# Kernel tuning notes

Hardware: AMD Instinct MI355X
Metric: run time of the kernel (lower is better)

The kernel has to match this reference:

```python
import jax, jax.numpy as jnp
import numpy as np

B, C, H, W = 4, 256, 64, 64
C8 = C // 8
MH, MW = 256, 256  # mask input resolution


def _conv(x, w, b, pad, dil=1):
    out = jax.lax.conv_general_dilated(
        x, w, window_strides=(1, 1),
        padding=[(pad, pad), (pad, pad)],
        rhs_dilation=(dil, dil),
        dimension_numbers=("NCHW", "OIHW", "NCHW"))
    return out + b[None, :, None, None]


def setup_inputs() -> dict:
    key = jax.random.key(0)
    ks = jax.random.split(key, 16)

    def w_init(k, shape):
        fan_in = shape[1] * shape[2] * shape[3]
        bound = 1.0 / np.sqrt(fan_in)
        return jax.random.uniform(k, shape, jnp.float32, -bound, bound)

    def b_init(k, n, fan_in):
        bound = 1.0 / np.sqrt(fan_in)
        return jax.random.uniform(k, (n,), jnp.float32, -bound, bound)

    return {
        "x": jax.random.normal(ks[0], (B, C, H, W), jnp.float32),
        "mask": jax.random.uniform(ks[1], (B, 1, MH, MW), jnp.float32),
        "w_ctx": w_init(ks[2], (C, C, 7, 7)),   "b_ctx": b_init(ks[3], C, C * 49),
        "w_wide": w_init(ks[4], (C, C, 5, 5)),  "b_wide": b_init(ks[5], C, C * 25),
        "w_comb": w_init(ks[6], (C, 2 * C, 1, 1)), "b_comb": b_init(ks[7], C, 2 * C),
        "w_q": w_init(ks[8], (C8, C, 1, 1)),    "b_q": b_init(ks[9], C8, C),
        "w_k": w_init(ks[10], (C8, C, 1, 1)),   "b_k": b_init(ks[11], C8, C),
        "w_v": w_init(ks[12], (C, C, 1, 1)),    "b_v": b_init(ks[13], C, C),
    }


def reference(x, mask, w_ctx, b_ctx, w_wide, b_wide, w_comb, b_comb,
              w_q, b_q, w_k, b_k, w_v, b_v):
    local_ctx = _conv(x, w_ctx, b_ctx, pad=3, dil=1)          # [B,C,H,W]
    wide_ctx = _conv(x, w_wide, b_wide, pad=6, dil=3)         # [B,C,H,W]
    multi = _conv(jnp.concatenate([local_ctx, wide_ctx], axis=1),
                  w_comb, b_comb, pad=0)                       # [B,C,H,W]

    b, c, h, w = multi.shape
    n = h * w
    q = _conv(multi, w_q, b_q, pad=0).reshape(b, C8, n)        # [B,C/8,N]
    k = _conv(multi, w_k, b_k, pad=0).reshape(b, C8, n)        # [B,C/8,N]
    v = _conv(multi, w_v, b_v, pad=0).reshape(b, c, n)         # [B,C,N]

    scores = jnp.einsum("bcm,bcn->bmn", q, k)                  # [B,N,N]
    attn = jax.nn.softmax(scores, axis=-1)
    out = jnp.einsum("bcn,bmn->bcm", v, attn).reshape(b, c, h, w)

    # nearest-neighbor resize of mask to (h, w), matching torch F.interpolate
    mh, mw = mask.shape[2], mask.shape[3]
    idx_h = (jnp.arange(h) * mh) // h
    idx_w = (jnp.arange(w) * mw) // w
    mask_r = mask[:, :, idx_h][:, :, :, idx_w]                 # [B,1,h,w]

    return out * (1.0 + mask_r)
```

## Files before the change

### kernel.cpp

```cpp
#include <hip/hip_runtime.h>
#include <math.h>

#define BB 4
#define CC 256
#define HH 64
#define WW 64
#define NN 4096

typedef _Float16 f16x8 __attribute__((ext_vector_type(8)));
typedef float f32x4 __attribute__((ext_vector_type(4)));

__device__ __forceinline__ void prep_pad(
    int blk, const float* __restrict__ x, _Float16* __restrict__ xpad)
{
  int pr = blk % 76;
  int b  = blk / 76;
  int ci = threadIdx.x;
  int r = pr - 6;
  _Float16* dst = xpad + (((size_t)b*76 + pr)*76)*256 + ci;
  if (r < 0 || r >= HH) {
    for (int pc = 0; pc < 76; ++pc) dst[(size_t)pc*256] = (_Float16)0.f;
  } else {
    #pragma unroll
    for (int pc = 0; pc < 6; ++pc) dst[(size_t)pc*256] = (_Float16)0.f;
    #pragma unroll
    for (int pc = 70; pc < 76; ++pc) dst[(size_t)pc*256] = (_Float16)0.f;
    const f32x4* s4 = (const f32x4*)(x + ((size_t)b*CC + ci)*NN + (size_t)r*WW);
    for (int q = 0; q < 16; ++q) {
      f32x4 v = s4[q];
      #pragma unroll
      for (int j = 0; j < 4; ++j)
        dst[(size_t)(6 + q*4 + j)*256] = (_Float16)v[j];
    }
  }
}

__device__ __forceinline__ void prep_wcvt(
    int co, const float* __restrict__ src, _Float16* __restrict__ dst, int T)
{
  int ci = threadIdx.x;
  const float* s = src + ((size_t)co*256 + ci)*T;
  for (int t = 0; t < T; ++t)
    dst[(size_t)t*65536 + co*256 + ci] = (_Float16)s[t];
}

__device__ __forceinline__ void prep_fcvt(
    int blk, const float* __restrict__ src, _Float16* __restrict__ dst, int n)
{
  int i = blk * 256 + threadIdx.x;
  if (i < n) dst[i] = (_Float16)src[i];
}

__global__ __launch_bounds__(256) void prep_kernel(
    const float* __restrict__ x,
    const float* __restrict__ w_ctx, const float* __restrict__ w_wide,
    const float* __restrict__ w_comb, const float* __restrict__ w_q,
    const float* __restrict__ w_k, const float* __restrict__ w_v,
    _Float16* __restrict__ xpad, _Float16* __restrict__ wb7,
    _Float16* __restrict__ wb5, _Float16* __restrict__ wcombH,
    _Float16* __restrict__ wqkH, _Float16* __restrict__ wvH)
{
  int blk = blockIdx.x;
  if      (blk < 304)  prep_pad(blk, x, xpad);
  else if (blk < 560)  prep_wcvt(blk - 304, w_ctx, wb7, 49);
  else if (blk < 816)  prep_wcvt(blk - 560, w_wide, wb5, 25);
  else if (blk < 1328) prep_fcvt(blk - 816, w_comb, wcombH, 131072);
  else if (blk < 1360) prep_fcvt(blk - 1328, w_q, wqkH, 8192);
  else if (blk < 1392) prep_fcvt(blk - 1360, w_k, wqkH + 8192, 8192);
  else                 prep_fcvt(blk - 1392, w_v, wvH, 65536);
}

template<int KS, int DIL>
__device__ __forceinline__ void conv_body(
    int ytile, int cot, int b,
    const _Float16* __restrict__ xpad, const _Float16* __restrict__ wb,
    const float* __restrict__ bias, _Float16* __restrict__ ctx_t, int c_off,
    char* xs)
{
  int y0 = ytile * 2;
  int tid = threadIdx.x;
  int lane = tid & 63;
  int wv = tid >> 6;
  int wco = wv >> 1;
  int wsp = wv & 1;
  int l15 = lane & 15;
  int lg  = lane >> 4;

  f32x4 acc[2][4];
  #pragma unroll
  for (int m = 0; m < 2; ++m)
    #pragma unroll
    for (int n = 0; n < 4; ++n) acc[m][n] = (f32x4){0.f, 0.f, 0.f, 0.f};

  for (int kh = 0; kh < KS; ++kh) {
    int prow = 6 + y0 + (kh - KS/2) * DIL;
    const uint4* src = (const uint4*)(xpad + (((size_t)b*76 + prow)*76)*256);
    __syncthreads();
    #pragma unroll
    for (int i = 0; i < 10; ++i) {
      int ch = tid + i*512;
      if (ch < 4864) {
        uint4 v = src[ch];
        int r = ch >> 5, cq = ch & 31;
        *(uint4*)(xs + r*512 + ((cq << 4) ^ ((r & 7) << 4))) = v;
      }
    }
    __syncthreads();
    for (int kw = 0; kw < KS; ++kw) {
      int dx = (kw - KS/2) * DIL;
      int tap = kh*KS + kw;
      const _Float16* wt = wb + ((size_t)tap << 16)
                              + ((size_t)(cot*128 + wco*32 + l15) << 8) + (lg << 3);
      #pragma unroll
      for (int half = 0; half < 2; ++half) {
        f16x8 w0[4], w1[4];
        #pragma unroll
        for (int kq = 0; kq < 4; ++kq) {
          int ks = half*4 + kq;
          w0[kq] = *(const f16x8*)(wt + ks*32);
          w1[kq] = *(const f16x8*)(wt + 16*256 + ks*32);
        }
        #pragma unroll
        for (int kq = 0; kq < 4; ++kq) {
          int ks = half*4 + kq;
          #pragma unroll
          for (int nf = 0; nf < 4; ++nf) {
            int r = wsp*76 + 6 + nf*16 + l15 + dx;
            f16x8 bf = *(const f16x8*)(xs + r*512 + ((ks*64 + (lg << 4)) ^ ((r & 7) << 4)));
            acc[0][nf] = __builtin_amdgcn_mfma_f32_16x16x32_f16(w0[kq], bf, acc[0][nf], 0, 0, 0);
            acc[1][nf] = __builtin_amdgcn_mfma_f32_16x16x32_f16(w1[kq], bf, acc[1][nf], 0, 0, 0);
          }
        }
      }
    }
  }

  __syncthreads();
  _Float16* ep = (_Float16*)xs;
  #pragma unroll
  for (int m = 0; m < 2; ++m)
    #pragma unroll
    for (int i = 0; i < 4; ++i) {
      int co_l = wco*32 + m*16 + lg*4 + i;
      float bs = bias[cot*128 + co_l];
      #pragma unroll
      for (int nf = 0; nf < 4; ++nf) {
        int n_l = wsp*64 + nf*16 + l15;
        ep[n_l*136 + co_l] = (_Float16)(acc[m][nf][i] + bs);
      }
    }
  __syncthreads();
  const int cbase = c_off + cot*128;
  #pragma unroll
  for (int it = 0; it < 4; ++it) {
    int idx = tid + it*512;
    int n_l = idx >> 4, q = idx & 15;
    f16x8 val = *(const f16x8*)(ep + n_l*136 + q*8);
    *(f16x8*)(ctx_t + ((size_t)b*4096 + (size_t)y0*64 + n_l)*512 + cbase + q*8) = val;
  }
}

__global__ __launch_bounds__(512, 4) void conv_both_kernel(
    const _Float16* __restrict__ xpad,
    const _Float16* __restrict__ wb7, const _Float16* __restrict__ wb5,
    const float* __restrict__ b7, const float* __restrict__ b5,
    _Float16* __restrict__ ctx_t)
{
  __shared__ __align__(16) char xs[2*76*512];
  int hw = blockIdx.x;
  int k = hw & 7, s = hw >> 3;
  if (s < 32)
    conv_body<7, 1>(s, k >> 2, k & 3, xpad, wb7, b7, ctx_t, 0, xs);
  else
    conv_body<5, 3>(s - 32, k & 1, k >> 1, xpad, wb5, b5, ctx_t, 256, xs);
}

template<int K, int O, int BIASMODE>
__global__ __launch_bounds__(64) void gemm_nmajor_kernel(
    const _Float16* __restrict__ A, const _Float16* __restrict__ Wt,
    const float* __restrict__ bias0, const float* __restrict__ bias1,
    _Float16* __restrict__ outh)
{
  int nt = blockIdx.x;
  int ot = blockIdx.y;
  int lane = threadIdx.x;
  int l15 = lane & 15, lg = lane >> 4;
  int n0 = nt*64, o0 = ot*64;
  f32x4 acc[4][4] = {};
  for (int k0 = 0; k0 < K; k0 += 32) {
    f16x8 a[4], bfr[4];
    #pragma unroll
    for (int f = 0; f < 4; ++f)
      a[f] = *(const f16x8*)(A + (size_t)(n0 + f*16 + l15)*K + k0 + lg*8);
    #pragma unroll
    for (int f = 0; f < 4; ++f)
      bfr[f] = *(const f16x8*)(Wt + (size_t)(o0 + f*16 + l15)*K + k0 + lg*8);
    #pragma unroll
    for (int i = 0; i < 4; ++i)
      #pragma unroll
      for (int j = 0; j < 4; ++j)
        acc[i][j] = __builtin_amdgcn_mfma_f32_16x16x32_f16(a[i], bfr[j], acc[i][j], 0, 0, 0);
  }
  #pragma unroll
  for (int i = 0; i < 4; ++i)
    #pragma unroll
    for (int j = 0; j < 4; ++j)
      #pragma unroll
      for (int r = 0; r < 4; ++r) {
        int n = n0 + i*16 + lg*4 + r;
        int o = o0 + j*16 + l15;
        float bs = (BIASMODE == 0) ? bias0[o] : (o < 32 ? bias0[o] : bias1[o - 32]);
        outh[(size_t)n*O + o] = (_Float16)(acc[i][j][r] + bs);
      }
}

__global__ __launch_bounds__(64) void gemm_v_kernel(
    const _Float16* __restrict__ M, const _Float16* __restrict__ Wv,
    const float* __restrict__ bias, _Float16* __restrict__ v)
{
  int nt = blockIdx.x;
  int ct = blockIdx.y;
  int lane = threadIdx.x;
  int l15 = lane & 15, lg = lane >> 4;
  int n0 = nt*64, c0 = ct*64;
  f32x4 acc[4][4] = {};
  for (int k0 = 0; k0 < 256; k0 += 32) {
    f16x8 a[4], bfr[4];
    #pragma unroll
    for (int f = 0; f < 4; ++f)
      a[f] = *(const f16x8*)(Wv + (size_t)(c0 + f*16 + l15)*256 + k0 + lg*8);
    #pragma unroll
    for (int f = 0; f < 4; ++f)
      bfr[f] = *(const f16x8*)(M + (size_t)(n0 + f*16 + l15)*256 + k0 + lg*8);
    #pragma unroll
    for (int i = 0; i < 4; ++i)
      #pragma unroll
      for (int j = 0; j < 4; ++j)
        acc[i][j] = __builtin_amdgcn_mfma_f32_16x16x32_f16(a[i], bfr[j], acc[i][j], 0, 0, 0);
  }
  #pragma unroll
  for (int i = 0; i < 4; ++i)
    #pragma unroll
    for (int j = 0; j < 4; ++j)
      #pragma unroll
      for (int r = 0; r < 4; ++r) {
        int c = c0 + i*16 + lg*4 + r;
        int n_abs = n0 + j*16 + l15;
        int b = n_abs >> 12, n = n_abs & 4095;
        v[((size_t)(b*256 + c))*4096 + n] = (_Float16)(acc[i][j][r] + bias[c]);
      }
}

__global__ __launch_bounds__(256) void attn_stats_kernel(
    const _Float16* __restrict__ qh,
    float* __restrict__ rowmaxP, float* __restrict__ rowsumP)
{
  int blk = blockIdx.x;
  int b = blk >> 7, mt = (blk >> 1) & 63, nh = blk & 1;
  int tid = threadIdx.x, lane = tid & 63, w = tid >> 6;
  int l15 = lane & 15, lg = lane >> 4;
  size_t bN = (size_t)b * 4096;
  int mrow = mt*64 + w*16;
  f16x8 ah = *(const f16x8*)(qh + (bN + mrow + l15)*64 + lg*8);
  float rm[4] = {-3e38f, -3e38f, -3e38f, -3e38f};
  float sm[4] = {0.f, 0.f, 0.f, 0.f};
  for (int n0 = nh*2048; n0 < nh*2048 + 2048; n0 += 16) {
    f16x8 bh = *(const f16x8*)(qh + (bN + n0 + l15)*64 + 32 + lg*8);
    f32x4 s = {};
    s = __builtin_amdgcn_mfma_f32_16x16x32_f16(ah, bh, s, 0, 0, 0);
    #pragma unroll
    for (int i = 0; i < 4; ++i) {
      float nm = fmaxf(rm[i], s[i]);
      sm[i] = sm[i]*__expf(rm[i] - nm) + __expf(s[i] - nm);
      rm[i] = nm;
    }
  }
  #pragma unroll
  for (int off = 1; off <= 8; off <<= 1) {
    #pragma unroll
    for (int i = 0; i < 4; ++i) {
      float rmo = __shfl_xor(rm[i], off);
      float smo = __shfl_xor(sm[i], off);
      float M = fmaxf(rm[i], rmo);
      sm[i] = sm[i]*__expf(rm[i] - M) + smo*__expf(rmo - M);
      rm[i] = M;
    }
  }
  if (l15 == 0) {
    #pragma unroll
    for (int i = 0; i < 4; ++i) {
      size_t idx = (size_t)nh*16384 + bN + mrow + lg*4 + i;
      rowmaxP[idx] = rm[i];
      rowsumP[idx] = sm[i];
    }
  }
}

__global__ __launch_bounds__(512) void attn_out_kernel(
    const _Float16* __restrict__ qh, const _Float16* __restrict__ v,
    const float* __restrict__ rowmaxP, const float* __restrict__ rowsumP,
    const float* __restrict__ mask, float* __restrict__ out)
{
  __shared__ union U {
    struct { __align__(16) _Float16 pl[64*40]; } s;
    float epi[256*68];
  } u;
  int blk = blockIdx.x;
  int b = blk >> 6, mt = blk & 63;
  int tid = threadIdx.x, lane = tid & 63, w = tid >> 6;
  int l15 = lane & 15, lg = lane >> 4;
  size_t bN = (size_t)b * 4096;
  int m0 = mt*64;

  int mf = w >> 1, nf2 = w & 1;
  f16x8 ah = *(const f16x8*)(qh + (bN + m0 + mf*16 + l15)*64 + lg*8);
  float rm[4], rsi[4];
  #pragma unroll
  for (int i = 0; i < 4; ++i) {
    size_t m = bN + m0 + mf*16 + lg*4 + i;
    float r0 = rowmaxP[m], r1 = rowmaxP[16384 + m];
    float s0 = rowsumP[m], s1 = rowsumP[16384 + m];
    float M = fmaxf(r0, r1);
    rm[i] = M;
    rsi[i] = 1.0f / (s0*__expf(r0 - M) + s1*__expf(r1 - M));
  }
  int mh = w >> 2, cw = (w & 3)*64;
  f32x4 acc[2][4] = {};
  const _Float16* vb = v + (size_t)b*256*4096;

  for (int n0 = 0; n0 < 4096; n0 += 32) {
    {
      f16x8 bh = *(const f16x8*)(qh + (bN + n0 + nf2*16 + l15)*64 + 32 + lg*8);
      f32x4 s = {};
      s = __builtin_amdgcn_mfma_f32_16x16x32_f16(ah, bh, s, 0, 0, 0);
      #pragma unroll
      for (int i = 0; i < 4; ++i) {
        float p = __expf(s[i] - rm[i]) * rsi[i];
        u.s.pl[(mf*16 + lg*4 + i)*40 + nf2*16 + l15] = (_Float16)p;
      }
    }
    __syncthreads();
    {
      f16x8 pa[2], pb[4];
      #pragma unroll
      for (int af = 0; af < 2; ++af)
        pa[af] = *(const f16x8*)(u.s.pl + (mh*32 + af*16 + l15)*40 + lg*8);
      #pragma unroll
      for (int bf = 0; bf < 4; ++bf)
        pb[bf] = *(const f16x8*)(vb + (size_t)(cw + bf*16 + l15)*4096 + n0 + lg*8);
      #pragma unroll
      for (int af = 0; af < 2; ++af)
        #pragma unroll
        for (int bf = 0; bf < 4; ++bf)
          acc[af][bf] = __builtin_amdgcn_mfma_f32_16x16x32_f16(pa[af], pb[bf], acc[af][bf], 0, 0, 0);
    }
    __syncthreads();
  }

  #pragma unroll
  for (int af = 0; af < 2; ++af)
    #pragma unroll
    for (int bf = 0; bf < 4; ++bf)
      #pragma unroll
      for (int r = 0; r < 4; ++r) {
        int c = cw + bf*16 + l15;
        int ml = mh*32 + af*16 + lg*4 + r;
        u.epi[c*68 + ml] = acc[af][bf][r];
      }
  __syncthreads();
  const float* mb = mask + (size_t)b*65536 + (size_t)(mt*4)*256;
  #pragma unroll
  for (int it = 0; it < 8; ++it) {
    int idx = tid + it*512;
    int c = idx >> 4, q = idx & 15;
    f32x4 val = *(const f32x4*)(u.epi + c*68 + q*4);
    f32x4 o4;
    #pragma unroll
    for (int jj = 0; jj < 4; ++jj) {
      int xcol = q*4 + jj;
      o4[jj] = val[jj] * (1.0f + mb[xcol*4]);
    }
    *(f32x4*)(out + ((size_t)b*256 + c)*4096 + m0 + q*4) = o4;
  }
}

extern "C" void kernel_launch(void* const* d_in, const int* in_sizes, int n_in,
                              void* d_out, int out_size, void* d_ws, size_t ws_size,
                              hipStream_t stream)
{
  (void)in_sizes; (void)n_in; (void)out_size; (void)ws_size;
  const float* x      = (const float*)d_in[0];
  const float* mask   = (const float*)d_in[1];
  const float* w_ctx  = (const float*)d_in[2];
  const float* b_ctx  = (const float*)d_in[3];
  const float* w_wide = (const float*)d_in[4];
  const float* b_wide = (const float*)d_in[5];
  const float* w_comb = (const float*)d_in[6];
  const float* b_comb = (const float*)d_in[7];
  const float* w_q    = (const float*)d_in[8];
  const float* b_q    = (const float*)d_in[9];
  const float* w_k    = (const float*)d_in[10];
  const float* b_k    = (const float*)d_in[11];
  const float* w_v    = (const float*)d_in[12];
  const float* b_v    = (const float*)d_in[13];
  float* out = (float*)d_out;

  float* ws = (float*)d_ws;
  _Float16* xpad    = (_Float16*)(ws);
  _Float16* wb7     = (_Float16*)(ws + 2957312);
  _Float16* wb5     = (_Float16*)(ws + 4562944);
  _Float16* ctx_t   = (_Float16*)(ws + 5382144);
  _Float16* wcombH  = (_Float16*)(ws + 9576448);
  _Float16* wqkH    = (_Float16*)(ws + 9641984);
  _Float16* wvH     = (_Float16*)(ws + 9650176);
  _Float16* multi_t = (_Float16*)(ws);
  _Float16* qkt_h   = (_Float16*)(ws + 2097152);
  float*    rowmaxP = ws + 2621440;
  float*    rowsumP = ws + 2654208;
  _Float16* vbuf    = (_Float16*)(ws + 5382144);

  prep_kernel<<<1648, 256, 0, stream>>>(x, w_ctx, w_wide, w_comb, w_q, w_k,
                                        w_v, xpad, wb7, wb5, wcombH, wqkH, wvH);

  conv_both_kernel<<<512, 512, 0, stream>>>(xpad, wb7, wb5, b_ctx, b_wide, ctx_t);

  gemm_nmajor_kernel<512, 256, 0><<<dim3(256, 4), 64, 0, stream>>>(
      ctx_t, wcombH, b_comb, nullptr, multi_t);
  gemm_nmajor_kernel<256, 64, 1><<<dim3(256, 1), 64, 0, stream>>>(
      multi_t, wqkH, b_q, b_k, qkt_h);
  gemm_v_kernel<<<dim3(256, 4), 64, 0, stream>>>(multi_t, wvH, b_v, vbuf);

  attn_stats_kernel<<<512, 256, 0, stream>>>(qkt_h, rowmaxP, rowsumP);
  attn_out_kernel<<<256, 512, 0, stream>>>(qkt_h, vbuf, rowmaxP, rowsumP,
                                           mask, out);
}
```

Measured before the change: 548.6 us.

## Shrink GEMM tiles, split softmax stats four ways, double attention K-step

The 1x1-conv GEMM kernels get smaller N tiles, launching 2-4x more single-wave blocks to raise occupancy on the many CUs. The softmax row-stats kernel splits each row's key range into four partitions instead of two, and the output kernel merges four partial max/sum pairs. The attention output loop now handles 64 keys per iteration with two MFMA K-steps, halving the number of barrier pairs. In exchange, smaller GEMM tiles reload the weights more often, and the larger P tile uses more LDS.

After: 550.6 us. About the same (+0.4%).

```diff
diff --git a/kernel.cpp b/kernel.cpp
--- a/kernel.cpp
+++ b/kernel.cpp
@@ -175,7 +175,7 @@
     conv_body<5, 3>(s - 32, k & 1, k >> 1, xpad, wb5, b5, ctx_t, 256, xs);
 }
 
-template<int K, int O, int BIASMODE>
+template<int K, int O, int BIASMODE, int MF>
 __global__ __launch_bounds__(64) void gemm_nmajor_kernel(
     const _Float16* __restrict__ A, const _Float16* __restrict__ Wt,
     const float* __restrict__ bias0, const float* __restrict__ bias1,
@@ -185,24 +185,24 @@
   int ot = blockIdx.y;
   int lane = threadIdx.x;
   int l15 = lane & 15, lg = lane >> 4;
-  int n0 = nt*64, o0 = ot*64;
-  f32x4 acc[4][4] = {};
+  int n0 = nt*(16*MF), o0 = ot*64;
+  f32x4 acc[MF][4] = {};
   for (int k0 = 0; k0 < K; k0 += 32) {
-    f16x8 a[4], bfr[4];
-    #pragma unroll
-    for (int f = 0; f < 4; ++f)
+    f16x8 a[MF], bfr[4];
+    #pragma unroll
+    for (int f = 0; f < MF; ++f)
       a[f] = *(const f16x8*)(A + (size_t)(n0 + f*16 + l15)*K + k0 + lg*8);
     #pragma unroll
     for (int f = 0; f < 4; ++f)
       bfr[f] = *(const f16x8*)(Wt + (size_t)(o0 + f*16 + l15)*K + k0 + lg*8);
     #pragma unroll
-    for (int i = 0; i < 4; ++i)
+    for (int i = 0; i < MF; ++i)
       #pragma unroll
       for (int j = 0; j < 4; ++j)
         acc[i][j] = __builtin_amdgcn_mfma_f32_16x16x32_f16(a[i], bfr[j], acc[i][j], 0, 0, 0);
   }
   #pragma unroll
-  for (int i = 0; i < 4; ++i)
+  for (int i = 0; i < MF; ++i)
     #pragma unroll
     for (int j = 0; j < 4; ++j)
       #pragma unroll
@@ -222,26 +222,26 @@
   int ct = blockIdx.y;
   int lane = threadIdx.x;
   int l15 = lane & 15, lg = lane >> 4;
-  int n0 = nt*64, c0 = ct*64;
-  f32x4 acc[4][4] = {};
+  int n0 = nt*32, c0 = ct*64;
+  f32x4 acc[4][2] = {};
   for (int k0 = 0; k0 < 256; k0 += 32) {
-    f16x8 a[4], bfr[4];
+    f16x8 a[4], bfr[2];
     #pragma unroll
     for (int f = 0; f < 4; ++f)
       a[f] = *(const f16x8*)(Wv + (size_t)(c0 + f*16 + l15)*256 + k0 + lg*8);
     #pragma unroll
-    for (int f = 0; f < 4; ++f)
+    for (int f = 0; f < 2; ++f)
       bfr[f] = *(const f16x8*)(M + (size_t)(n0 + f*16 + l15)*256 + k0 + lg*8);
     #pragma unroll
     for (int i = 0; i < 4; ++i)
       #pragma unroll
-      for (int j = 0; j < 4; ++j)
+      for (int j = 0; j < 2; ++j)
         acc[i][j] = __builtin_amdgcn_mfma_f32_16x16x32_f16(a[i], bfr[j], acc[i][j], 0, 0, 0);
   }
   #pragma unroll
   for (int i = 0; i < 4; ++i)
     #pragma unroll
-    for (int j = 0; j < 4; ++j)
+    for (int j = 0; j < 2; ++j)
       #pragma unroll
       for (int r = 0; r < 4; ++r) {
         int c = c0 + i*16 + lg*4 + r;
@@ -256,7 +256,7 @@
     float* __restrict__ rowmaxP, float* __restrict__ rowsumP)
 {
   int blk = blockIdx.x;
-  int b = blk >> 7, mt = (blk >> 1) & 63, nh = blk & 1;
+  int b = blk >> 8, mt = (blk >> 2) & 63, nh = blk & 3;
   int tid = threadIdx.x, lane = tid & 63, w = tid >> 6;
   int l15 = lane & 15, lg = lane >> 4;
   size_t bN = (size_t)b * 4096;
@@ -264,7 +264,7 @@
   f16x8 ah = *(const f16x8*)(qh + (bN + mrow + l15)*64 + lg*8);
   float rm[4] = {-3e38f, -3e38f, -3e38f, -3e38f};
   float sm[4] = {0.f, 0.f, 0.f, 0.f};
-  for (int n0 = nh*2048; n0 < nh*2048 + 2048; n0 += 16) {
+  for (int n0 = nh*1024; n0 < nh*1024 + 1024; n0 += 16) {
     f16x8 bh = *(const f16x8*)(qh + (bN + n0 + l15)*64 + 32 + lg*8);
     f32x4 s = {};
     s = __builtin_amdgcn_mfma_f32_16x16x32_f16(ah, bh, s, 0, 0, 0);
@@ -302,7 +302,7 @@
     const float* __restrict__ mask, float* __restrict__ out)
 {
   __shared__ union U {
-    struct { __align__(16) _Float16 pl[64*40]; } s;
+    struct { __align__(16) _Float16 pl[64*72]; } s;
     float epi[256*68];
   } u;
   int blk = blockIdx.x;
@@ -319,40 +319,52 @@
   for (int i = 0; i < 4; ++i) {
     size_t m = bN + m0 + mf*16 + lg*4 + i;
     float r0 = rowmaxP[m], r1 = rowmaxP[16384 + m];
-    float s0 = rowsumP[m], s1 = rowsumP[16384 + m];
-    float M = fmaxf(r0, r1);
+    float r2 = rowmaxP[32768 + m], r3 = rowmaxP[49152 + m];
+    float M = fmaxf(fmaxf(r0, r1), fmaxf(r2, r3));
+    float ssum = rowsumP[m]         * __expf(r0 - M)
+               + rowsumP[16384 + m] * __expf(r1 - M)
+               + rowsumP[32768 + m] * __expf(r2 - M)
+               + rowsumP[49152 + m] * __expf(r3 - M);
     rm[i] = M;
-    rsi[i] = 1.0f / (s0*__expf(r0 - M) + s1*__expf(r1 - M));
+    rsi[i] = 1.0f / ssum;
   }
   int mh = w >> 2, cw = (w & 3)*64;
   f32x4 acc[2][4] = {};
   const _Float16* vb = v + (size_t)b*256*4096;
 
-  for (int n0 = 0; n0 < 4096; n0 += 32) {
-    {
-      f16x8 bh = *(const f16x8*)(qh + (bN + n0 + nf2*16 + l15)*64 + 32 + lg*8);
+  for (int n0 = 0; n0 < 4096; n0 += 64) {
+    #pragma unroll
+    for (int nn = 0; nn < 2; ++nn) {
+      int nl = nf2*16 + nn*32;
+      f16x8 bh = *(const f16x8*)(qh + (bN + n0 + nl + l15)*64 + 32 + lg*8);
       f32x4 s = {};
       s = __builtin_amdgcn_mfma_f32_16x16x32_f16(ah, bh, s, 0, 0, 0);
       #pragma unroll
       for (int i = 0; i < 4; ++i) {
         float p = __expf(s[i] - rm[i]) * rsi[i];
-        u.s.pl[(mf*16 + lg*4 + i)*40 + nf2*16 + l15] = (_Float16)p;
+        u.s.pl[(mf*16 + lg*4 + i)*72 + nl + l15] = (_Float16)p;
       }
     }
     __syncthreads();
     {
-      f16x8 pa[2], pb[4];
-      #pragma unroll
-      for (int af = 0; af < 2; ++af)
-        pa[af] = *(const f16x8*)(u.s.pl + (mh*32 + af*16 + l15)*40 + lg*8);
-      #pragma unroll
-      for (int bf = 0; bf < 4; ++bf)
-        pb[bf] = *(const f16x8*)(vb + (size_t)(cw + bf*16 + l15)*4096 + n0 + lg*8);
+      f16x8 pa[2][2], pb[4][2];
       #pragma unroll
       for (int af = 0; af < 2; ++af)
         #pragma unroll
-        for (int bf = 0; bf < 4; ++bf)
-          acc[af][bf] = __builtin_amdgcn_mfma_f32_16x16x32_f16(pa[af], pb[bf], acc[af][bf], 0, 0, 0);
+        for (int ks = 0; ks < 2; ++ks)
+          pa[af][ks] = *(const f16x8*)(u.s.pl + (mh*32 + af*16 + l15)*72 + ks*32 + lg*8);
+      #pragma unroll
+      for (int bf = 0; bf < 4; ++bf)
+        #pragma unroll
+        for (int ks = 0; ks < 2; ++ks)
+          pb[bf][ks] = *(const f16x8*)(vb + (size_t)(cw + bf*16 + l15)*4096 + n0 + ks*32 + lg*8);
+      #pragma unroll
+      for (int ks = 0; ks < 2; ++ks)
+        #pragma unroll
+        for (int af = 0; af < 2; ++af)
+          #pragma unroll
+          for (int bf = 0; bf < 4; ++bf)
+            acc[af][bf] = __builtin_amdgcn_mfma_f32_16x16x32_f16(pa[af][ks], pb[bf][ks], acc[af][bf], 0, 0, 0);
     }
     __syncthreads();
   }
@@ -416,7 +428,7 @@
   _Float16* multi_t = (_Float16*)(ws);
   _Float16* qkt_h   = (_Float16*)(ws + 2097152);
   float*    rowmaxP = ws + 2621440;
-  float*    rowsumP = ws + 2654208;
+  float*    rowsumP = ws + 2686976;
   _Float16* vbuf    = (_Float16*)(ws + 5382144);
 
   prep_kernel<<<1648, 256, 0, stream>>>(x, w_ctx, w_wide, w_comb, w_q, w_k,
@@ -424,13 +436,13 @@
 
   conv_both_kernel<<<512, 512, 0, stream>>>(xpad, wb7, wb5, b_ctx, b_wide, ctx_t);
 
-  gemm_nmajor_kernel<512, 256, 0><<<dim3(256, 4), 64, 0, stream>>>(
+  gemm_nmajor_kernel<512, 256, 0, 2><<<dim3(512, 4), 64, 0, stream>>>(
       ctx_t, wcombH, b_comb, nullptr, multi_t);
-  gemm_nmajor_kernel<256, 64, 1><<<dim3(256, 1), 64, 0, stream>>>(
+  gemm_nmajor_kernel<256, 64, 1, 1><<<dim3(1024, 1), 64, 0, stream>>>(
       multi_t, wqkH, b_q, b_k, qkt_h);
-  gemm_v_kernel<<<dim3(256, 4), 64, 0, stream>>>(multi_t, wvH, b_v, vbuf);
-
-  attn_stats_kernel<<<512, 256, 0, stream>>>(qkt_h, rowmaxP, rowsumP);
+  gemm_v_kernel<<<dim3(512, 4), 64, 0, stream>>>(multi_t, wvH, b_v, vbuf);
+
+  attn_stats_kernel<<<1024, 256, 0, stream>>>(qkt_h, rowmaxP, rowsumP);
   attn_out_kernel<<<256, 512, 0, stream>>>(qkt_h, vbuf, rowmaxP, rowsumP,
                                            mask, out);
 }
```

## Fold 1x1 combine conv into conv weights and stage V tiles in LDS

Applied to the files above, without the earlier changes.

Premultiplies the 7x7 and dilated 5x5 conv weights by their halves of the 1x1 combine weights, and folds all biases into one combined bias. The two convs now each write a 256-channel partial of multi, and the qk and v GEMMs sum the two partials when they load them. This removes the separate combine GEMM and the 512-channel ctx intermediate. The attention output kernel also stages each V tile in shared memory, so its global loads are coalesced instead of strided. The costs are an extra weight-fusion GEMM every call, two partial buffers to read, fp16 rounding of the fused weights and of the partial sums, and a larger LDS footprint in the attention kernel.

New measurement: 529.4 us. 1.04x faster.

```diff
diff --git a/kernel.cpp b/kernel.cpp
--- a/kernel.cpp
+++ b/kernel.cpp
@@ -70,11 +70,66 @@
   else                 prep_fcvt(blk - 1392, w_v, wvH, 65536);
 }
 
-template<int KS, int DIL>
+__global__ __launch_bounds__(64) void wfuse_kernel(
+    const _Float16* __restrict__ wb7, const _Float16* __restrict__ wb5,
+    const _Float16* __restrict__ wcombH,
+    _Float16* __restrict__ wf7, _Float16* __restrict__ wf5)
+{
+  int t = blockIdx.x;
+  int ct = blockIdx.y;
+  int lane = threadIdx.x;
+  int l15 = lane & 15, lg = lane >> 4;
+  const _Float16* wb; _Float16* wf; int part;
+  if (t < 49) { wb = wb7 + (size_t)t*65536; wf = wf7 + (size_t)t*65536; part = 0; }
+  else        { wb = wb5 + (size_t)(t-49)*65536; wf = wf5 + (size_t)(t-49)*65536; part = 1; }
+  int co0 = ct*64;
+  for (int cit = 0; cit < 4; ++cit) {
+    int ci0 = cit*64;
+    f32x4 acc[4][4] = {};
+    for (int k0 = 0; k0 < 256; k0 += 32) {
+      f16x8 a[4], bfr[4];
+      #pragma unroll
+      for (int f = 0; f < 4; ++f)
+        a[f] = *(const f16x8*)(wcombH + (size_t)(co0 + f*16 + l15)*512 + part*256 + k0 + lg*8);
+      #pragma unroll
+      for (int f = 0; f < 4; ++f)
+        #pragma unroll
+        for (int j = 0; j < 8; ++j)
+          bfr[f][j] = wb[(size_t)(k0 + lg*8 + j)*256 + ci0 + f*16 + l15];
+      #pragma unroll
+      for (int i = 0; i < 4; ++i)
+        #pragma unroll
+        for (int j = 0; j < 4; ++j)
+          acc[i][j] = __builtin_amdgcn_mfma_f32_16x16x32_f16(a[i], bfr[j], acc[i][j], 0, 0, 0);
+    }
+    #pragma unroll
+    for (int i = 0; i < 4; ++i)
+      #pragma unroll
+      for (int j = 0; j < 4; ++j)
+        #pragma unroll
+        for (int r = 0; r < 4; ++r)
+          wf[(size_t)(co0 + i*16 + lg*4 + r)*256 + ci0 + j*16 + l15] = (_Float16)acc[i][j][r];
+  }
+}
+
+__global__ __launch_bounds__(256) void mbias_kernel(
+    const float* __restrict__ w_comb, const float* __restrict__ b_comb,
+    const float* __restrict__ b_ctx, const float* __restrict__ b_wide,
+    float* __restrict__ mbias)
+{
+  int o = threadIdx.x;
+  float s = b_comb[o];
+  const float* wr = w_comb + (size_t)o*512;
+  for (int m = 0; m < 256; ++m) s = fmaf(wr[m], b_ctx[m], s);
+  for (int m = 0; m < 256; ++m) s = fmaf(wr[256 + m], b_wide[m], s);
+  mbias[o] = s;
+}
+
+template<int KS, int DIL, bool BIAS>
 __device__ __forceinline__ void conv_body(
     int ytile, int cot, int b,
     const _Float16* __restrict__ xpad, const _Float16* __restrict__ wb,
-    const float* __restrict__ bias, _Float16* __restrict__ ctx_t, int c_off,
+    const float* __restrict__ bias, _Float16* __restrict__ outp,
     char* xs)
 {
   int y0 = ytile * 2;
@@ -142,7 +197,7 @@
     #pragma unroll
     for (int i = 0; i < 4; ++i) {
       int co_l = wco*32 + m*16 + lg*4 + i;
-      float bs = bias[cot*128 + co_l];
+      float bs = BIAS ? bias[cot*128 + co_l] : 0.f;
       #pragma unroll
       for (int nf = 0; nf < 4; ++nf) {
         int n_l = wsp*64 + nf*16 + l15;
@@ -150,98 +205,95 @@
       }
     }
   __syncthreads();
-  const int cbase = c_off + cot*128;
+  const int cbase = cot*128;
   #pragma unroll
   for (int it = 0; it < 4; ++it) {
     int idx = tid + it*512;
     int n_l = idx >> 4, q = idx & 15;
     f16x8 val = *(const f16x8*)(ep + n_l*136 + q*8);
-    *(f16x8*)(ctx_t + ((size_t)b*4096 + (size_t)y0*64 + n_l)*512 + cbase + q*8) = val;
+    *(f16x8*)(outp + ((size_t)b*4096 + (size_t)y0*64 + n_l)*256 + cbase + q*8) = val;
   }
 }
 
 __global__ __launch_bounds__(512, 4) void conv_both_kernel(
     const _Float16* __restrict__ xpad,
-    const _Float16* __restrict__ wb7, const _Float16* __restrict__ wb5,
-    const float* __restrict__ b7, const float* __restrict__ b5,
-    _Float16* __restrict__ ctx_t)
+    const _Float16* __restrict__ wf7, const _Float16* __restrict__ wf5,
+    const float* __restrict__ mbias,
+    _Float16* __restrict__ m7, _Float16* __restrict__ m5)
 {
   __shared__ __align__(16) char xs[2*76*512];
   int hw = blockIdx.x;
   int k = hw & 7, s = hw >> 3;
   if (s < 32)
-    conv_body<7, 1>(s, k >> 2, k & 3, xpad, wb7, b7, ctx_t, 0, xs);
+    conv_body<7, 1, true >(s, k >> 2, k & 3, xpad, wf7, mbias, m7, xs);
   else
-    conv_body<5, 3>(s - 32, k & 1, k >> 1, xpad, wb5, b5, ctx_t, 256, xs);
-}
-
-template<int K, int O, int BIASMODE>
-__global__ __launch_bounds__(64) void gemm_nmajor_kernel(
-    const _Float16* __restrict__ A, const _Float16* __restrict__ Wt,
+    conv_body<5, 3, false>(s - 32, k & 1, k >> 1, xpad, wf5, mbias, m5, xs);
+}
+
+__global__ __launch_bounds__(64) void gemm_qk_kernel(
+    const _Float16* __restrict__ A, const _Float16* __restrict__ A2,
+    const _Float16* __restrict__ Wt,
     const float* __restrict__ bias0, const float* __restrict__ bias1,
     _Float16* __restrict__ outh)
 {
   int nt = blockIdx.x;
-  int ot = blockIdx.y;
   int lane = threadIdx.x;
   int l15 = lane & 15, lg = lane >> 4;
-  int n0 = nt*64, o0 = ot*64;
-  f32x4 acc[4][4] = {};
-  for (int k0 = 0; k0 < K; k0 += 32) {
-    f16x8 a[4], bfr[4];
+  int n0 = nt*16;
+  f32x4 acc[4] = {};
+  for (int k0 = 0; k0 < 256; k0 += 32) {
+    size_t aoff = (size_t)(n0 + l15)*256 + k0 + lg*8;
+    f16x8 a = *(const f16x8*)(A + aoff) + *(const f16x8*)(A2 + aoff);
+    f16x8 bfr[4];
     #pragma unroll
     for (int f = 0; f < 4; ++f)
-      a[f] = *(const f16x8*)(A + (size_t)(n0 + f*16 + l15)*K + k0 + lg*8);
-    #pragma unroll
-    for (int f = 0; f < 4; ++f)
-      bfr[f] = *(const f16x8*)(Wt + (size_t)(o0 + f*16 + l15)*K + k0 + lg*8);
-    #pragma unroll
-    for (int i = 0; i < 4; ++i)
-      #pragma unroll
-      for (int j = 0; j < 4; ++j)
-        acc[i][j] = __builtin_amdgcn_mfma_f32_16x16x32_f16(a[i], bfr[j], acc[i][j], 0, 0, 0);
-  }
-  #pragma unroll
-  for (int i = 0; i < 4; ++i)
+      bfr[f] = *(const f16x8*)(Wt + (size_t)(f*16 + l15)*256 + k0 + lg*8);
     #pragma unroll
     for (int j = 0; j < 4; ++j)
-      #pragma unroll
-      for (int r = 0; r < 4; ++r) {
-        int n = n0 + i*16 + lg*4 + r;
-        int o = o0 + j*16 + l15;
-        float bs = (BIASMODE == 0) ? bias0[o] : (o < 32 ? bias0[o] : bias1[o - 32]);
-        outh[(size_t)n*O + o] = (_Float16)(acc[i][j][r] + bs);
-      }
+      acc[j] = __builtin_amdgcn_mfma_f32_16x16x32_f16(a, bfr[j], acc[j], 0, 0, 0);
+  }
+  #pragma unroll
+  for (int j = 0; j < 4; ++j)
+    #pragma unroll
+    for (int r = 0; r < 4; ++r) {
+      int n = n0 + lg*4 + r;
+      int o = j*16 + l15;
+      float bs = (o < 32) ? bias0[o] : bias1[o - 32];
+      outh[(size_t)n*64 + o] = (_Float16)(acc[j][r] + bs);
+    }
 }
 
 __global__ __launch_bounds__(64) void gemm_v_kernel(
-    const _Float16* __restrict__ M, const _Float16* __restrict__ Wv,
+    const _Float16* __restrict__ M, const _Float16* __restrict__ M2,
+    const _Float16* __restrict__ Wv,
     const float* __restrict__ bias, _Float16* __restrict__ v)
 {
   int nt = blockIdx.x;
   int ct = blockIdx.y;
   int lane = threadIdx.x;
   int l15 = lane & 15, lg = lane >> 4;
-  int n0 = nt*64, c0 = ct*64;
-  f32x4 acc[4][4] = {};
+  int n0 = nt*32, c0 = ct*64;
+  f32x4 acc[4][2] = {};
   for (int k0 = 0; k0 < 256; k0 += 32) {
-    f16x8 a[4], bfr[4];
+    f16x8 a[4], bfr[2];
     #pragma unroll
     for (int f = 0; f < 4; ++f)
       a[f] = *(const f16x8*)(Wv + (size_t)(c0 + f*16 + l15)*256 + k0 + lg*8);
     #pragma unroll
-    for (int f = 0; f < 4; ++f)
-      bfr[f] = *(const f16x8*)(M + (size_t)(n0 + f*16 + l15)*256 + k0 + lg*8);
+    for (int f = 0; f < 2; ++f) {
+      size_t moff = (size_t)(n0 + f*16 + l15)*256 + k0 + lg*8;
+      bfr[f] = *(const f16x8*)(M + moff) + *(const f16x8*)(M2 + moff);
+    }
     #pragma unroll
     for (int i = 0; i < 4; ++i)
       #pragma unroll
-      for (int j = 0; j < 4; ++j)
+      for (int j = 0; j < 2; ++j)
         acc[i][j] = __builtin_amdgcn_mfma_f32_16x16x32_f16(a[i], bfr[j], acc[i][j], 0, 0, 0);
   }
   #pragma unroll
   for (int i = 0; i < 4; ++i)
     #pragma unroll
-    for (int j = 0; j < 4; ++j)
+    for (int j = 0; j < 2; ++j)
       #pragma unroll
       for (int r = 0; r < 4; ++r) {
         int c = c0 + i*16 + lg*4 + r;
@@ -302,7 +354,7 @@
     const float* __restrict__ mask, float* __restrict__ out)
 {
   __shared__ union U {
-    struct { __align__(16) _Float16 pl[64*40]; } s;
+    struct { __align__(16) _Float16 vs[256*40]; __align__(16) _Float16 pl[64*40]; } s;
     float epi[256*68];
   } u;
   int blk = blockIdx.x;
@@ -329,6 +381,12 @@
   const _Float16* vb = v + (size_t)b*256*4096;
 
   for (int n0 = 0; n0 < 4096; n0 += 32) {
+    #pragma unroll
+    for (int it = 0; it < 2; ++it) {
+      int idx = tid + it*512;
+      int c = idx >> 2, q = idx & 3;
+      *(f16x8*)(u.s.vs + c*40 + q*8) = *(const f16x8*)(vb + (size_t)c*4096 + n0 + q*8);
+    }
     {
       f16x8 bh = *(const f16x8*)(qh + (bN + n0 + nf2*16 + l15)*64 + 32 + lg*8);
       f32x4 s = {};
@@ -347,7 +405,7 @@
         pa[af] = *(const f16x8*)(u.s.pl + (mh*32 + af*16 + l15)*40 + lg*8);
       #pragma unroll
       for (int bf = 0; bf < 4; ++bf)
-        pb[bf] = *(const f16x8*)(vb + (size_t)(cw + bf*16 + l15)*4096 + n0 + lg*8);
+        pb[bf] = *(const f16x8*)(u.s.vs + (cw + bf*16 + l15)*40 + lg*8);
       #pragma unroll
       for (int af = 0; af < 2; ++af)
         #pragma unroll
@@ -409,26 +467,28 @@
   _Float16* xpad    = (_Float16*)(ws);
   _Float16* wb7     = (_Float16*)(ws + 2957312);
   _Float16* wb5     = (_Float16*)(ws + 4562944);
-  _Float16* ctx_t   = (_Float16*)(ws + 5382144);
-  _Float16* wcombH  = (_Float16*)(ws + 9576448);
-  _Float16* wqkH    = (_Float16*)(ws + 9641984);
-  _Float16* wvH     = (_Float16*)(ws + 9650176);
-  _Float16* multi_t = (_Float16*)(ws);
-  _Float16* qkt_h   = (_Float16*)(ws + 2097152);
-  float*    rowmaxP = ws + 2621440;
-  float*    rowsumP = ws + 2654208;
-  _Float16* vbuf    = (_Float16*)(ws + 5382144);
+  _Float16* wcombH  = (_Float16*)(ws + 5382144);
+  _Float16* wqkH    = (_Float16*)(ws + 5447680);
+  _Float16* wvH     = (_Float16*)(ws + 5455872);
+  _Float16* wf7     = (_Float16*)(ws + 5488640);
+  _Float16* wf5     = (_Float16*)(ws + 7094272);
+  float*    mbias   = ws + 7913472;
+  _Float16* m7      = (_Float16*)(ws + 7913728);
+  _Float16* m5      = (_Float16*)(ws + 10010880);
+  _Float16* qkt_h   = (_Float16*)(ws);
+  float*    rowmaxP = ws + 524288;
+  float*    rowsumP = ws + 557056;
+  _Float16* vbuf    = (_Float16*)(ws + 589824);
 
   prep_kernel<<<1648, 256, 0, stream>>>(x, w_ctx, w_wide, w_comb, w_q, w_k,
                                         w_v, xpad, wb7, wb5, wcombH, wqkH, wvH);
-
-  conv_both_kernel<<<512, 512, 0, stream>>>(xpad, wb7, wb5, b_ctx, b_wide, ctx_t);
-
-  gemm_nmajor_kernel<512, 256, 0><<<dim3(256, 4), 64, 0, stream>>>(
-      ctx_t, wcombH, b_comb, nullptr, multi_t);
-  gemm_nmajor_kernel<256, 64, 1><<<dim3(256, 1), 64, 0, stream>>>(
-      multi_t, wqkH, b_q, b_k, qkt_h);
-  gemm_v_kernel<<<dim3(256, 4), 64, 0, stream>>>(multi_t, wvH, b_v, vbuf);
+  wfuse_kernel<<<dim3(74, 4), 64, 0, stream>>>(wb7, wb5, wcombH, wf7, wf5);
+  mbias_kernel<<<1, 256, 0, stream>>>(w_comb, b_comb, b_ctx, b_wide, mbias);
+
+  conv_both_kernel<<<512, 512, 0, stream>>>(xpad, wf7, wf5, mbias, m7, m5);
+
+  gemm_qk_kernel<<<1024, 64, 0, stream>>>(m7, m5, wqkH, b_q, b_k, qkt_h);
+  gemm_v_kernel<<<dim3(512, 4), 64, 0, stream>>>(m7, m5, wvH, b_v, vbuf);
 
   attn_stats_kernel<<<512, 256, 0, stream>>>(qkt_h, rowmaxP, rowsumP);
   attn_out_kernel<<<256, 512, 0, stream>>>(qkt_h, vbuf, rowmaxP, rowsumP,
```
